# Kernel optimization log

Measured on AMD Instinct MI355X. Metric: run time of the kernel, lower is better.

The kernel has to match this reference:

```python
import jax, jax.numpy as jnp
import numpy as np
from jax import lax

N = 100000
E = 1600000
IN_C = 128
HID = 128
OUT_C = 64
NUM_CLASSES = 40
BN_EPS = 1e-5


def gcn_conv(x, row, col, W, b):
    # x: [N, F_in] -> [N, F_out]; PyG GCNConv: self-loops + sym normalization
    h = x @ W                                   # [N, F_out]
    loops = jnp.arange(N, dtype=row.dtype)
    r = jnp.concatenate([row, loops])           # [E+N]
    c = jnp.concatenate([col, loops])
    ones = jnp.ones(r.shape[0], dtype=x.dtype)
    deg = jax.ops.segment_sum(ones, c, num_segments=N)
    dinv = jnp.where(deg > 0, lax.rsqrt(deg), jnp.zeros_like(deg))
    norm = dinv[r] * dinv[c]                    # [E+N]
    msg = h[r] * norm[:, None]                  # gather + scale  [E+N, F_out]
    out = jax.ops.segment_sum(msg, c, num_segments=N)
    return out + b


def setup_inputs() -> dict:
    key = jax.random.key(0)
    ks = jax.random.split(key, 16)
    def glorot(k, shape):
        lim = float(np.sqrt(6.0 / (shape[0] + shape[1])))
        return jax.random.uniform(k, shape, jnp.float32, -lim, lim)
    x = jax.random.normal(ks[0], (N, IN_C), jnp.float32)
    edge_index = jax.random.randint(ks[1], (2, E), 0, N, jnp.int64)
    return {
        "x": x,
        "edge_index": edge_index,
        "w1": glorot(ks[2], (IN_C, HID)), "b1": jnp.zeros((HID,), jnp.float32),
        "w2": glorot(ks[3], (HID, HID)), "b2": jnp.zeros((HID,), jnp.float32),
        "bn_gamma": jnp.ones((HID,), jnp.float32), "bn_beta": jnp.zeros((HID,), jnp.float32),
        "bn_mean": jnp.zeros((HID,), jnp.float32), "bn_var": jnp.ones((HID,), jnp.float32),
        "cls_w": glorot(ks[4], (HID, OUT_C)), "cls_b": jnp.zeros((OUT_C,), jnp.float32),
        "sim_w": glorot(ks[5], (HID, NUM_CLASSES)), "sim_b": jnp.zeros((NUM_CLASSES,), jnp.float32),
        "hom_w": glorot(ks[6], (HID, 1)), "hom_b": jnp.zeros((1,), jnp.float32),
        "ent_w": glorot(ks[7], (HID, 1)), "ent_b": jnp.zeros((1,), jnp.float32),
    }


def reference(x, edge_index, w1, b1, w2, b2, bn_gamma, bn_beta, bn_mean, bn_var,
              cls_w, cls_b, sim_w, sim_b, hom_w, hom_b, ent_w, ent_b):
    row, col = edge_index[0], edge_index[1]
    # layer 1: GCNConv -> BN (eval) -> ReLU (dropout is identity in eval)
    h = gcn_conv(x, row, col, w1, b1)
    h = (h - bn_mean) * lax.rsqrt(bn_var + BN_EPS) * bn_gamma + bn_beta
    h = jax.nn.relu(h)
    # layer 2
    h = gcn_conv(h, row, col, w2, b2)
    main_out = jax.nn.log_softmax(h @ cls_w + cls_b, axis=1)
    sim_out = jax.nn.softmax(h @ sim_w + sim_b, axis=1)
    hom_out = jax.nn.sigmoid((h @ hom_w + hom_b)[:, 0])
    ent_out = jax.nn.sigmoid((h @ ent_w + ent_b)[:, 0])
    return (main_out, sim_out, hom_out, ent_out)
```

## Files before the change

### kernel.cpp

```cpp
#include <hip/hip_runtime.h>
#include <hip/hip_bf16.h>
#include <math.h>

#define N_NODES 100000
#define N_EDGES 1600000
#define F 128
#define OUT_C 64
#define NUM_CLASSES 40
#define BN_EPS 1e-5f

#define NBUCK 782
#define BCAP 4096
#define FILL_BLOCKS 512
#define EPB ((N_EDGES + FILL_BLOCKS - 1) / FILL_BLOCKS)
#define FILL_ITERS 13

typedef __hip_bfloat16 bf16;
typedef __attribute__((ext_vector_type(8))) short bf16x8;
typedef __attribute__((ext_vector_type(4))) float f32x4;

#define PW1 0
#define PB1 16384
#define PW2 16512
#define PB2 32896
#define PGAMMA 33024
#define PBETA 33152
#define PMEAN 33280
#define PVAR 33408
#define PCLSW 33536
#define PCLSB 41728
#define PSIMW 41792
#define PSIMB 46912
#define PHOMW 46952
#define PHOMB 47080
#define PENTW 47081
#define PENTB 47209
#define PRAW_TOTAL 47210
#define PFW 47232
#define PFB 63616
#define PTOTAL 63744

__device__ __forceinline__ float uasf(unsigned u) { return __uint_as_float(u); }
__device__ __forceinline__ unsigned f2bu(float f) {
    bf16 h = __float2bfloat16(f);
    return (unsigned)*(unsigned short*)&h;
}

__global__ void detect_kernel(const void* __restrict__ x, const void* __restrict__ ei,
                              int* __restrict__ flags) {
    if (blockIdx.x != 0) return;
    int t = threadIdx.x & 63;
    const unsigned* xw = (const unsigned*)x;
    unsigned w = xw[t];
    unsigned e = (w >> 23) & 0xFFu;
    bool vote = (w == 0u || (e >= 90u && e <= 160u));
    unsigned long long m1 = __ballot(vote);
    const unsigned* ew = (const unsigned*)ei;
    bool zo = (ew[2 * t + 1] == 0u);
    unsigned long long m2 = __ballot(zo);
    if (t == 0) {
        flags[0] = (__popcll(m1) >= 48) ? 1 : 0;
        flags[1] = (__popcll(m2) >= 60) ? 1 : 0;
    }
}

struct ParamSegs {
    const void* src[16];
    int dst[16];
};

__global__ void cvtparams_kernel(ParamSegs segs, float* __restrict__ params,
                                 const int* __restrict__ flags) {
    int idx = blockIdx.x * 256 + threadIdx.x;
    if (idx >= PRAW_TOTAL) return;
    int k = 0;
#pragma unroll
    for (int s = 1; s < 16; s++)
        if (idx >= segs.dst[s]) k = s;
    int rel = idx - segs.dst[k];
    const void* sp = segs.src[k];
    float v = flags[0] ? ((const float*)sp)[rel]
                       : __bfloat162float(((const bf16*)sp)[rel]);
    params[idx] = v;
}

__device__ __forceinline__ int load_edge(const int* __restrict__ ei, int which, int i, int i64) {
    size_t elem = (size_t)which * N_EDGES + (size_t)i;
    return i64 ? ei[elem * 2] : ei[elem];
}

__global__ __launch_bounds__(256) void fill2_kernel(const int* __restrict__ ei,
                                                    int* __restrict__ bcur,
                                                    int* __restrict__ srcBuck,
                                                    const int* __restrict__ flags) {
    __shared__ int hist[NBUCK];
    __shared__ int gbase[NBUCK];
    __shared__ int lcur[NBUCK];
    int blk = blockIdx.x;
    int t = threadIdx.x;
    int i64 = flags[1];
    int e0 = blk * EPB;
    int ecnt = N_EDGES - e0;
    if (ecnt > EPB) ecnt = EPB;
    for (int i = t; i < NBUCK; i += 256) hist[i] = 0;
    __syncthreads();
    int ccache[FILL_ITERS];
#pragma unroll
    for (int it = 0; it < FILL_ITERS; ++it) {
        int i = t + it * 256;
        int c = -1;
        if (i < ecnt) {
            c = load_edge(ei, 1, e0 + i, i64);
            atomicAdd(&hist[c >> 7], 1);
        }
        ccache[it] = c;
    }
    __syncthreads();
    for (int i = t; i < NBUCK; i += 256) {
        int c = hist[i];
        gbase[i] = (c > 0) ? atomicAdd(&bcur[i], c) : 0;
        lcur[i] = 0;
    }
    __syncthreads();
#pragma unroll
    for (int it = 0; it < FILL_ITERS; ++it) {
        int i = t + it * 256;
        if (i < ecnt) {
            int c = ccache[it];
            int r = load_edge(ei, 0, e0 + i, i64);
            int b = c >> 7;
            int p = gbase[b] + atomicAdd(&lcur[b], 1);
            if (p < BCAP) srcBuck[b * BCAP + p] = ((c & 127) << 17) | r;
        }
    }
}

__global__ __launch_bounds__(512) void presort_kernel(int* __restrict__ srcBuck,
                                                      const int* __restrict__ bcur,
                                                      int* __restrict__ doffG,
                                                      int* __restrict__ dcntG,
                                                      float* __restrict__ dinv) {
    __shared__ int raw[BCAP];
    __shared__ int sorted[BCAP];
    __shared__ int dcnt[128], doff[128], dcur[128];
    int b = blockIdx.x;
    int t = threadIdx.x;
    int cnt = bcur[b];
    if (cnt > BCAP) cnt = BCAP;
    if (t < 128) dcnt[t] = 0;
    __syncthreads();
    for (int i = t; i < cnt; i += 512) {
        int e = srcBuck[b * BCAP + i];
        raw[i] = e;
        atomicAdd(&dcnt[e >> 17], 1);
    }
    __syncthreads();
    if (t < 128) doff[t] = dcnt[t];
    __syncthreads();
    for (int d = 1; d < 128; d <<= 1) {
        int add = 0;
        if (t < 128 && t >= d) add = doff[t - d];
        __syncthreads();
        if (t < 128) doff[t] += add;
        __syncthreads();
    }
    if (t < 128) {
        doff[t] -= dcnt[t];
        dcur[t] = 0;
    }
    __syncthreads();
    for (int i = t; i < cnt; i += 512) {
        int e = raw[i];
        int d = e >> 17;
        int r = atomicAdd(&dcur[d], 1);
        sorted[doff[d] + r] = e & 0x1FFFF;
    }
    __syncthreads();
    for (int i = t; i < cnt; i += 512) srcBuck[b * BCAP + i] = sorted[i];
    if (t < 128) {
        doffG[(b << 7) + t] = doff[t];
        dcntG[(b << 7) + t] = dcnt[t];
        int n = (b << 7) + t;
        if (n < N_NODES) dinv[n] = rsqrtf((float)(dcnt[t] + 1));
    }
}

__global__ void cvtx_kernel(const void* __restrict__ x, const float* __restrict__ dinv,
                            unsigned short* __restrict__ B16, const int* __restrict__ flags) {
    int i4 = blockIdx.x * blockDim.x + threadIdx.x;
    if (i4 >= N_NODES * F / 4) return;
    int n = i4 >> 5;
    float d = dinv[n];
    float v0, v1, v2, v3;
    if (flags[0]) {
        float4 v = ((const float4*)x)[i4];
        v0 = v.x; v1 = v.y; v2 = v.z; v3 = v.w;
    } else {
        uint2 u = ((const uint2*)x)[i4];
        v0 = uasf(u.x << 16);
        v1 = uasf(u.x & 0xFFFF0000u);
        v2 = uasf(u.y << 16);
        v3 = uasf(u.y & 0xFFFF0000u);
    }
    uint2 o;
    o.x = f2bu(v0 * d) | (f2bu(v1 * d) << 16);
    o.y = f2bu(v2 * d) | (f2bu(v3 * d) << 16);
    ((uint2*)B16)[i4] = o;
}

__device__ __forceinline__ float headw(const float* __restrict__ p, int j, int c) {
    if (c < OUT_C) return p[PCLSW + j * OUT_C + c];
    if (c < OUT_C + NUM_CLASSES) return p[PSIMW + j * NUM_CLASSES + (c - OUT_C)];
    if (c == 104) return p[PHOMW + j];
    if (c == 105) return p[PENTW + j];
    return 0.f;
}

__global__ void fusew_kernel(float* __restrict__ params) {
    int idx = blockIdx.x * 256 + threadIdx.x;
    int k = idx >> 7;
    int c = idx & 127;
    float s = 0.f;
    for (int j = 0; j < 128; j++) s += params[PW2 + k * 128 + j] * headw(params, j, c);
    params[PFW + k * 128 + c] = s;
    if (k == 0) {
        float b = 0.f;
        for (int j = 0; j < 128; j++) b += params[PB2 + j] * headw(params, j, c);
        if (c < OUT_C) b += params[PCLSB + c];
        else if (c < OUT_C + NUM_CLASSES) b += params[PSIMB + c - OUT_C];
        else if (c == 104) b += params[PHOMB];
        else if (c == 105) b += params[PENTB];
        params[PFB + c] = b;
    }
}

__global__ void wcvt_kernel(const float* __restrict__ params, unsigned short* __restrict__ wt) {
    int idx = blockIdx.x * 256 + threadIdx.x;
    if (idx >= 32768) return;
    int which = idx >> 14;
    int local = idx & 16383;
    int n = local >> 7;
    int k = local & 127;
    int ksrc = which ? ((k & 7) * 16 + (k >> 3)) : k;
    float v = params[(which ? PFW : PW1) + ksrc * 128 + n];
    wt[(which << 14) + n * 128 + k] = (unsigned short)f2bu(v);
}

#define ACC8(u)                                \
    do {                                       \
        a[0] += uasf((u).x << 16);             \
        a[1] += uasf((u).x & 0xFFFF0000u);     \
        a[2] += uasf((u).y << 16);             \
        a[3] += uasf((u).y & 0xFFFF0000u);     \
        a[4] += uasf((u).z << 16);             \
        a[5] += uasf((u).z & 0xFFFF0000u);     \
        a[6] += uasf((u).w << 16);             \
        a[7] += uasf((u).w & 0xFFFF0000u);     \
    } while (0)

__global__ __launch_bounds__(512) void aggh_kernel(const unsigned short* __restrict__ IN16,
                                                   unsigned short* __restrict__ OUT16,
                                                   const int* __restrict__ srcBuck,
                                                   const int* __restrict__ doffG,
                                                   const int* __restrict__ dcntG,
                                                   const float* __restrict__ dinv,
                                                   int* __restrict__ wcnt) {
    __shared__ int sIdx[BCAP];
    __shared__ int sdoff[128], sdcnt[128];
    __shared__ int sb, sh;
    int t = threadIdx.x;
    if (t == 0) {
        unsigned xcc;
        asm volatile("s_getreg_b32 %0, hwreg(HW_REG_XCC_ID)" : "=s"(xcc));
        int half = (xcc >> 2) & 1;
        int idx = atomicAdd(&wcnt[half], 1);
        if (idx >= NBUCK) {
            half ^= 1;
            idx = atomicAdd(&wcnt[half], 1);
        }
        sb = idx;
        sh = half;
    }
    __syncthreads();
    int b = sb, h = sh;
    if (t < 128) {
        sdoff[t] = doffG[(b << 7) + t];
        sdcnt[t] = dcntG[(b << 7) + t];
    }
    __syncthreads();
    int cnt = sdoff[127] + sdcnt[127];
    for (int i = t; i < cnt; i += 512) sIdx[i] = srcBuck[b * BCAP + i];
    __syncthreads();

    int g8 = t >> 3;
    int hoff = h * 64 + ((t & 7) << 3);
    int base = b << 7;
    for (int d = g8; d < 128; d += 64) {
        int n = base + d;
        if (n >= N_NODES) break;
        float a[8] = {0.f, 0.f, 0.f, 0.f, 0.f, 0.f, 0.f, 0.f};
        {
            uint4 u = *(const uint4*)(IN16 + ((size_t)n << 7) + hoff);
            ACC8(u);
        }
        int o = sdoff[d], k = sdcnt[d];
        int j = 0;
        for (; j + 8 <= k; j += 8) {
            int s0 = sIdx[o + j + 0], s1 = sIdx[o + j + 1];
            int s2 = sIdx[o + j + 2], s3 = sIdx[o + j + 3];
            int s4 = sIdx[o + j + 4], s5 = sIdx[o + j + 5];
            int s6 = sIdx[o + j + 6], s7 = sIdx[o + j + 7];
            uint4 u0 = *(const uint4*)(IN16 + ((size_t)s0 << 7) + hoff);
            uint4 u1 = *(const uint4*)(IN16 + ((size_t)s1 << 7) + hoff);
            uint4 u2 = *(const uint4*)(IN16 + ((size_t)s2 << 7) + hoff);
            uint4 u3 = *(const uint4*)(IN16 + ((size_t)s3 << 7) + hoff);
            uint4 u4 = *(const uint4*)(IN16 + ((size_t)s4 << 7) + hoff);
            uint4 u5 = *(const uint4*)(IN16 + ((size_t)s5 << 7) + hoff);
            uint4 u6 = *(const uint4*)(IN16 + ((size_t)s6 << 7) + hoff);
            uint4 u7 = *(const uint4*)(IN16 + ((size_t)s7 << 7) + hoff);
            ACC8(u0);
            ACC8(u1);
            ACC8(u2);
            ACC8(u3);
            ACC8(u4);
            ACC8(u5);
            ACC8(u6);
            ACC8(u7);
        }
        for (; j + 4 <= k; j += 4) {
            int s0 = sIdx[o + j + 0], s1 = sIdx[o + j + 1];
            int s2 = sIdx[o + j + 2], s3 = sIdx[o + j + 3];
            uint4 u0 = *(const uint4*)(IN16 + ((size_t)s0 << 7) + hoff);
            uint4 u1 = *(const uint4*)(IN16 + ((size_t)s1 << 7) + hoff);
            uint4 u2 = *(const uint4*)(IN16 + ((size_t)s2 << 7) + hoff);
            uint4 u3 = *(const uint4*)(IN16 + ((size_t)s3 << 7) + hoff);
            ACC8(u0);
            ACC8(u1);
            ACC8(u2);
            ACC8(u3);
        }
        for (; j < k; j++) {
            int s0 = sIdx[o + j];
            uint4 u0 = *(const uint4*)(IN16 + ((size_t)s0 << 7) + hoff);
            ACC8(u0);
        }
        float dn = dinv[n];
        uint4 pk;
        pk.x = f2bu(a[0] * dn) | (f2bu(a[1] * dn) << 16);
        pk.y = f2bu(a[2] * dn) | (f2bu(a[3] * dn) << 16);
        pk.z = f2bu(a[4] * dn) | (f2bu(a[5] * dn) << 16);
        pk.w = f2bu(a[6] * dn) | (f2bu(a[7] * dn) << 16);
        *(uint4*)(OUT16 + ((size_t)n << 7) + hoff) = pk;
    }
}

__global__ __launch_bounds__(256) void gemm_mfma_kernel(
    const unsigned short* __restrict__ A16, const unsigned short* __restrict__ Wt,
    unsigned short* __restrict__ outB, void* __restrict__ out,
    const float* __restrict__ params, const float* __restrict__ dinv, int mode,
    const int* __restrict__ flags) {
    __shared__ float sS[128], sO[128], sFB[128];
    int t = threadIdx.x;
    if (t < 128) {
        if (mode) {
            float s = rsqrtf(params[PVAR + t] + BN_EPS) * params[PGAMMA + t];
            sS[t] = s;
            sO[t] = params[PB1 + t] * s + (params[PBETA + t] - params[PMEAN + t] * s);
        } else {
            sFB[t] = params[PFB + t];
        }
    }
    __syncthreads();
    int wave = t >> 6, lane = t & 63, m16 = lane & 15, quad = lane >> 4;
    int rowbase = blockIdx.x * 64 + wave * 16;
    int rA = rowbase + m16;
    if (rA >= N_NODES) rA = N_NODES - 1;
    const size_t abase = (size_t)rA * 128 + (quad << 3);

    f32x4 acc[8];
#pragma unroll
    for (int ct = 0; ct < 8; ct++) acc[ct] = (f32x4){0.f, 0.f, 0.f, 0.f};

#pragma unroll
    for (int kk = 0; kk < 4; kk++) {
        bf16x8 af = *(const bf16x8*)(A16 + abase + kk * 32);
#pragma unroll
        for (int ct = 0; ct < 8; ct++) {
            bf16x8 bfr = *(const bf16x8*)(Wt + (size_t)((ct * 16 + m16) * 128) + kk * 32 + (quad << 3));
            acc[ct] = __builtin_amdgcn_mfma_f32_16x16x32_bf16(af, bfr, acc[ct], 0, 0, 0);
        }
    }

    int r0 = rowbase + quad * 4;
    if (mode) {
        float sc[8], of[8];
#pragma unroll
        for (int ct = 0; ct < 8; ct++) {
            sc[ct] = sS[ct * 16 + m16];
            of[ct] = sO[ct * 16 + m16];
        }
#pragma unroll
        for (int reg = 0; reg < 4; reg++) {
            int gr = r0 + reg;
            if (gr >= N_NODES) continue;
            float dn = dinv[gr];
            unsigned pk[4];
#pragma unroll
            for (int i = 0; i < 4; i++) {
                float v0 = fmaxf(acc[2 * i][reg] * sc[2 * i] + of[2 * i], 0.f) * dn;
                float v1 = fmaxf(acc[2 * i + 1][reg] * sc[2 * i + 1] + of[2 * i + 1], 0.f) * dn;
                pk[i] = f2bu(v0) | (f2bu(v1) << 16);
            }
            *(uint4*)(outB + (size_t)gr * 128 + (m16 << 3)) = make_uint4(pk[0], pk[1], pk[2], pk[3]);
        }
    } else {
        int isf = flags[0];
        const size_t OFF_SIM = (size_t)N_NODES * OUT_C;
        const size_t OFF_HOM = OFF_SIM + (size_t)N_NODES * NUM_CLASSES;
        const size_t OFF_ENT = OFF_HOM + (size_t)N_NODES;
        float* outf = (float*)out;
        bf16* outb = (bf16*)out;
        float fb[8];
#pragma unroll
        for (int ct = 0; ct < 8; ct++) fb[ct] = sFB[ct * 16 + m16];
#define STORE_OUT(idx, v)                        \
    do {                                         \
        if (isf) outf[(idx)] = (v);              \
        else outb[(idx)] = __float2bfloat16(v);  \
    } while (0)
#pragma unroll
        for (int reg = 0; reg < 4; reg++) {
            int gr = r0 + reg;
            bool vrow = (gr < N_NODES);
            float v[8];
#pragma unroll
            for (int ct = 0; ct < 8; ct++) v[ct] = acc[ct][reg] + fb[ct];
            float m = fmaxf(fmaxf(v[0], v[1]), fmaxf(v[2], v[3]));
            m = fmaxf(m, __shfl_xor(m, 1));
            m = fmaxf(m, __shfl_xor(m, 2));
            m = fmaxf(m, __shfl_xor(m, 4));
            m = fmaxf(m, __shfl_xor(m, 8));
            float S = __expf(v[0] - m) + __expf(v[1] - m) + __expf(v[2] - m) + __expf(v[3] - m);
            S += __shfl_xor(S, 1);
            S += __shfl_xor(S, 2);
            S += __shfl_xor(S, 4);
            S += __shfl_xor(S, 8);
            float lS = m + __logf(S);
            if (vrow) {
#pragma unroll
                for (int ct = 0; ct < 4; ct++)
                    STORE_OUT((size_t)gr * OUT_C + ct * 16 + m16, v[ct] - lS);
            }
            bool has6 = (m16 < 8);
            float s4 = v[4], s5 = v[5], s6 = has6 ? v[6] : -INFINITY;
            float m2 = fmaxf(fmaxf(s4, s5), s6);
            m2 = fmaxf(m2, __shfl_xor(m2, 1));
            m2 = fmaxf(m2, __shfl_xor(m2, 2));
            m2 = fmaxf(m2, __shfl_xor(m2, 4));
            m2 = fmaxf(m2, __shfl_xor(m2, 8));
            float e4 = __expf(s4 - m2), e5 = __expf(s5 - m2), e6 = has6 ? __expf(s6 - m2) : 0.f;
            float S2 = e4 + e5 + e6;
            S2 += __shfl_xor(S2, 1);
            S2 += __shfl_xor(S2, 2);
            S2 += __shfl_xor(S2, 4);
            S2 += __shfl_xor(S2, 8);
            float rS2 = 1.f / S2;
            if (vrow) {
                STORE_OUT(OFF_SIM + (size_t)gr * NUM_CLASSES + m16, e4 * rS2);
                STORE_OUT(OFF_SIM + (size_t)gr * NUM_CLASSES + 16 + m16, e5 * rS2);
                if (has6) STORE_OUT(OFF_SIM + (size_t)gr * NUM_CLASSES + 32 + m16, e6 * rS2);
                if (m16 == 8) STORE_OUT(OFF_HOM + gr, 1.f / (1.f + __expf(-v[6])));
                if (m16 == 9) STORE_OUT(OFF_ENT + gr, 1.f / (1.f + __expf(-v[6])));
            }
        }
#undef STORE_OUT
    }
}

extern "C" void kernel_launch(void* const* d_in, const int* in_sizes, int n_in,
                              void* d_out, int out_size, void* d_ws, size_t ws_size,
                              hipStream_t stream) {
    const void* x = d_in[0];
    const int* ei = (const int*)d_in[1];

    char* ws = (char*)d_ws;
    size_t o = 0;
    auto alloc = [&](size_t bytes) {
        size_t r = o;
        o = (o + bytes + 255) & ~(size_t)255;
        return r;
    };
    char* RA = ws + alloc((size_t)51 * 1024 * 1024);
    char* RB = ws + alloc((size_t)26 * 1024 * 1024);
    float* params = (float*)(ws + alloc((size_t)PTOTAL * 4));
    unsigned short* wt = (unsigned short*)(ws + alloc(65536));
    float* dinv = (float*)(ws + alloc((size_t)N_NODES * 4));
    int* doffG = (int*)(ws + alloc((size_t)NBUCK * 128 * 4));
    int* dcntG = (int*)(ws + alloc((size_t)NBUCK * 128 * 4));
    int* bcur = (int*)(ws + alloc((size_t)(NBUCK + 8) * 4));
    int* wcnt = (int*)(ws + alloc(256));
    int* flags = (int*)(ws + alloc(256));

    int* srcBuck = (int*)RA;
    unsigned short* B16 = (unsigned short*)(RA + 13u * 1024 * 1024);
    unsigned short* G16 = (unsigned short*)RB;

    detect_kernel<<<1, 64, 0, stream>>>(x, ei, flags);
    hipMemsetAsync(bcur, 0, (size_t)((char*)wcnt + 256 - (char*)bcur), stream);

    ParamSegs segs;
    const int srcIdx[16] = {2, 3, 4, 5, 6, 7, 8, 9, 10, 11, 12, 13, 14, 15, 16, 17};
    const int dsts[16] = {PW1, PB1, PW2, PB2, PGAMMA, PBETA, PMEAN, PVAR,
                          PCLSW, PCLSB, PSIMW, PSIMB, PHOMW, PHOMB, PENTW, PENTB};
    for (int k = 0; k < 16; k++) {
        segs.src[k] = d_in[srcIdx[k]];
        segs.dst[k] = dsts[k];
    }
    cvtparams_kernel<<<(PRAW_TOTAL + 255) / 256, 256, 0, stream>>>(segs, params, flags);
    fusew_kernel<<<64, 256, 0, stream>>>(params);
    wcvt_kernel<<<128, 256, 0, stream>>>(params, wt);

    fill2_kernel<<<FILL_BLOCKS, 256, 0, stream>>>(ei, bcur, srcBuck, flags);
    presort_kernel<<<NBUCK, 512, 0, stream>>>(srcBuck, bcur, doffG, dcntG, dinv);
    cvtx_kernel<<<(N_NODES * F / 4 + 255) / 256, 256, 0, stream>>>(x, dinv, B16, flags);

    const int gemmGrid = (N_NODES + 63) / 64;

    aggh_kernel<<<2 * NBUCK, 512, 0, stream>>>(B16, G16, srcBuck, doffG, dcntG, dinv, wcnt);
    gemm_mfma_kernel<<<gemmGrid, 256, 0, stream>>>(G16, wt, B16, nullptr, params, dinv, 1, flags);
    aggh_kernel<<<2 * NBUCK, 512, 0, stream>>>(B16, G16, srcBuck, doffG, dcntG, dinv, wcnt + 2);
    gemm_mfma_kernel<<<gemmGrid, 256, 0, stream>>>(G16, wt + 16384, nullptr, d_out, params, dinv, 0, flags);
}
```

Measured before the change: 438.3 us.

## Fuse whole GCN pipeline into one cooperative persistent kernel with grid syncs

Replaces the chain of about ten kernel launches with one cooperative kernel of 256 blocks × 512 threads. Stages (detect, param convert, bucket fill, presort, weight fuse, x convert, two aggregation and GEMM phases) are separated by grid.sync, and the aggregation loop becomes persistent work-stealing. The goal is to remove launch gaps and inter-kernel drain. The trade-off is fewer resident blocks than the old grids, occupancy limits from large shared memory under the launch bounds, and the cost of the grid barriers. The old multi-kernel path is kept as a fallback if the cooperative launch fails.

New measurement: 1.166 ms. +166.0%, slower.

```diff
diff --git a/kernel.cpp b/kernel.cpp
--- a/kernel.cpp
+++ b/kernel.cpp
@@ -1,6 +1,9 @@
 #include <hip/hip_runtime.h>
+#include <hip/hip_cooperative_groups.h>
 #include <hip/hip_bf16.h>
 #include <math.h>
+
+namespace cg = cooperative_groups;
 
 #define N_NODES 100000
 #define N_EDGES 1600000
@@ -11,9 +14,15 @@
 
 #define NBUCK 782
 #define BCAP 4096
+
 #define FILL_BLOCKS 512
 #define EPB ((N_EDGES + FILL_BLOCKS - 1) / FILL_BLOCKS)
 #define FILL_ITERS 13
+
+#define GB 256
+#define BT 512
+#define MEPB ((N_EDGES + GB - 1) / GB)
+#define MFITERS ((MEPB + BT - 1) / BT)
 
 typedef __hip_bfloat16 bf16;
 typedef __attribute__((ext_vector_type(8))) short bf16x8;
@@ -40,10 +49,458 @@
 #define PFB 63616
 #define PTOTAL 63744
 
+struct ParamSegs {
+    const void* src[16];
+    int dst[16];
+};
+
 __device__ __forceinline__ float uasf(unsigned u) { return __uint_as_float(u); }
 __device__ __forceinline__ unsigned f2bu(float f) {
     bf16 h = __float2bfloat16(f);
     return (unsigned)*(unsigned short*)&h;
+}
+__device__ __forceinline__ int load_edge(const int* __restrict__ ei, int which, int i, int i64) {
+    size_t elem = (size_t)which * N_EDGES + (size_t)i;
+    return i64 ? ei[elem * 2] : ei[elem];
+}
+__device__ __forceinline__ float headw(const float* __restrict__ p, int j, int c) {
+    if (c < OUT_C) return p[PCLSW + j * OUT_C + c];
+    if (c < OUT_C + NUM_CLASSES) return p[PSIMW + j * NUM_CLASSES + (c - OUT_C)];
+    if (c == 104) return p[PHOMW + j];
+    if (c == 105) return p[PENTW + j];
+    return 0.f;
+}
+
+#define ACC8(u)                                \
+    do {                                       \
+        a[0] += uasf((u).x << 16);             \
+        a[1] += uasf((u).x & 0xFFFF0000u);     \
+        a[2] += uasf((u).y << 16);             \
+        a[3] += uasf((u).y & 0xFFFF0000u);     \
+        a[4] += uasf((u).z << 16);             \
+        a[5] += uasf((u).z & 0xFFFF0000u);     \
+        a[6] += uasf((u).w << 16);             \
+        a[7] += uasf((u).w & 0xFFFF0000u);     \
+    } while (0)
+
+__device__ void agg_phase(const unsigned short* __restrict__ IN16,
+                          unsigned short* __restrict__ OUT16,
+                          const int* __restrict__ srcBuck, const int* __restrict__ doffG,
+                          const int* __restrict__ dcntG, const float* __restrict__ dinv,
+                          int* __restrict__ wpair, int t, int* __restrict__ sIdx,
+                          int* __restrict__ sdoff, int* __restrict__ sdcnt,
+                          volatile int* __restrict__ sCtl, int nthreads) {
+    int g8 = t >> 3;
+    int lo8 = (t & 7) << 3;
+    int ng = nthreads >> 3;
+    for (;;) {
+        if (t == 0) {
+            unsigned xcc;
+            asm volatile("s_getreg_b32 %0, hwreg(HW_REG_XCC_ID)" : "=s"(xcc));
+            int half = (xcc >> 2) & 1;
+            int idx = atomicAdd(&wpair[half], 1);
+            if (idx >= NBUCK) {
+                half ^= 1;
+                idx = atomicAdd(&wpair[half], 1);
+            }
+            sCtl[0] = (idx < NBUCK) ? idx : -1;
+            sCtl[1] = half;
+        }
+        __syncthreads();
+        int b = sCtl[0], h = sCtl[1];
+        if (b < 0) break;
+        if (t < 128) {
+            sdoff[t] = doffG[(b << 7) + t];
+            sdcnt[t] = dcntG[(b << 7) + t];
+        }
+        __syncthreads();
+        int cnt = sdoff[127] + sdcnt[127];
+        for (int i = t; i < cnt; i += nthreads) sIdx[i] = srcBuck[b * BCAP + i];
+        __syncthreads();
+        int hoff = h * 64 + lo8;
+        int base = b << 7;
+        for (int d = g8; d < 128; d += ng) {
+            int n = base + d;
+            if (n >= N_NODES) break;
+            float a[8] = {0.f, 0.f, 0.f, 0.f, 0.f, 0.f, 0.f, 0.f};
+            {
+                uint4 u = *(const uint4*)(IN16 + ((size_t)n << 7) + hoff);
+                ACC8(u);
+            }
+            int o = sdoff[d], k = sdcnt[d];
+            int j = 0;
+            for (; j + 8 <= k; j += 8) {
+                int s0 = sIdx[o + j + 0], s1 = sIdx[o + j + 1];
+                int s2 = sIdx[o + j + 2], s3 = sIdx[o + j + 3];
+                int s4 = sIdx[o + j + 4], s5 = sIdx[o + j + 5];
+                int s6 = sIdx[o + j + 6], s7 = sIdx[o + j + 7];
+                uint4 u0 = *(const uint4*)(IN16 + ((size_t)s0 << 7) + hoff);
+                uint4 u1 = *(const uint4*)(IN16 + ((size_t)s1 << 7) + hoff);
+                uint4 u2 = *(const uint4*)(IN16 + ((size_t)s2 << 7) + hoff);
+                uint4 u3 = *(const uint4*)(IN16 + ((size_t)s3 << 7) + hoff);
+                uint4 u4 = *(const uint4*)(IN16 + ((size_t)s4 << 7) + hoff);
+                uint4 u5 = *(const uint4*)(IN16 + ((size_t)s5 << 7) + hoff);
+                uint4 u6 = *(const uint4*)(IN16 + ((size_t)s6 << 7) + hoff);
+                uint4 u7 = *(const uint4*)(IN16 + ((size_t)s7 << 7) + hoff);
+                ACC8(u0);
+                ACC8(u1);
+                ACC8(u2);
+                ACC8(u3);
+                ACC8(u4);
+                ACC8(u5);
+                ACC8(u6);
+                ACC8(u7);
+            }
+            for (; j + 4 <= k; j += 4) {
+                int s0 = sIdx[o + j + 0], s1 = sIdx[o + j + 1];
+                int s2 = sIdx[o + j + 2], s3 = sIdx[o + j + 3];
+                uint4 u0 = *(const uint4*)(IN16 + ((size_t)s0 << 7) + hoff);
+                uint4 u1 = *(const uint4*)(IN16 + ((size_t)s1 << 7) + hoff);
+                uint4 u2 = *(const uint4*)(IN16 + ((size_t)s2 << 7) + hoff);
+                uint4 u3 = *(const uint4*)(IN16 + ((size_t)s3 << 7) + hoff);
+                ACC8(u0);
+                ACC8(u1);
+                ACC8(u2);
+                ACC8(u3);
+            }
+            for (; j < k; j++) {
+                int s0 = sIdx[o + j];
+                uint4 u0 = *(const uint4*)(IN16 + ((size_t)s0 << 7) + hoff);
+                ACC8(u0);
+            }
+            float dn = dinv[n];
+            uint4 pk;
+            pk.x = f2bu(a[0] * dn) | (f2bu(a[1] * dn) << 16);
+            pk.y = f2bu(a[2] * dn) | (f2bu(a[3] * dn) << 16);
+            pk.z = f2bu(a[4] * dn) | (f2bu(a[5] * dn) << 16);
+            pk.w = f2bu(a[6] * dn) | (f2bu(a[7] * dn) << 16);
+            *(uint4*)(OUT16 + ((size_t)n << 7) + hoff) = pk;
+        }
+        __syncthreads();
+    }
+}
+
+__device__ void gemm_tile(const unsigned short* __restrict__ A16,
+                          const unsigned short* __restrict__ Wt,
+                          unsigned short* __restrict__ outB, void* __restrict__ out,
+                          const float* __restrict__ dinv, int mode, int isf,
+                          const float* __restrict__ sF1, const float* __restrict__ sF2,
+                          int t, int rowbase0) {
+    int w = t >> 6, lane = t & 63, m16 = lane & 15, quad = lane >> 4;
+    int rowbase = rowbase0 + w * 16;
+    int rA = rowbase + m16;
+    if (rA >= N_NODES) rA = N_NODES - 1;
+    const size_t abase = (size_t)rA * 128 + (quad << 3);
+
+    f32x4 acc[8];
+#pragma unroll
+    for (int ct = 0; ct < 8; ct++) acc[ct] = (f32x4){0.f, 0.f, 0.f, 0.f};
+#pragma unroll
+    for (int kk = 0; kk < 4; kk++) {
+        bf16x8 af = *(const bf16x8*)(A16 + abase + kk * 32);
+#pragma unroll
+        for (int ct = 0; ct < 8; ct++) {
+            bf16x8 bfr =
+                *(const bf16x8*)(Wt + (size_t)((ct * 16 + m16) * 128) + kk * 32 + (quad << 3));
+            acc[ct] = __builtin_amdgcn_mfma_f32_16x16x32_bf16(af, bfr, acc[ct], 0, 0, 0);
+        }
+    }
+
+    int r0 = rowbase + quad * 4;
+    if (mode) {
+        float sc[8], of[8];
+#pragma unroll
+        for (int ct = 0; ct < 8; ct++) {
+            sc[ct] = sF1[ct * 16 + m16];
+            of[ct] = sF2[ct * 16 + m16];
+        }
+#pragma unroll
+        for (int reg = 0; reg < 4; reg++) {
+            int gr = r0 + reg;
+            if (gr >= N_NODES) continue;
+            float dn = dinv[gr];
+            unsigned pk[4];
+#pragma unroll
+            for (int i = 0; i < 4; i++) {
+                float v0 = fmaxf(acc[2 * i][reg] * sc[2 * i] + of[2 * i], 0.f) * dn;
+                float v1 = fmaxf(acc[2 * i + 1][reg] * sc[2 * i + 1] + of[2 * i + 1], 0.f) * dn;
+                pk[i] = f2bu(v0) | (f2bu(v1) << 16);
+            }
+            *(uint4*)(outB + (size_t)gr * 128 + (m16 << 3)) = make_uint4(pk[0], pk[1], pk[2], pk[3]);
+        }
+    } else {
+        const size_t OFF_SIM = (size_t)N_NODES * OUT_C;
+        const size_t OFF_HOM = OFF_SIM + (size_t)N_NODES * NUM_CLASSES;
+        const size_t OFF_ENT = OFF_HOM + (size_t)N_NODES;
+        float* outf = (float*)out;
+        bf16* outb = (bf16*)out;
+        float fb[8];
+#pragma unroll
+        for (int ct = 0; ct < 8; ct++) fb[ct] = sF1[ct * 16 + m16];
+#define STORE_OUT(idx, v)                        \
+    do {                                         \
+        if (isf) outf[(idx)] = (v);              \
+        else outb[(idx)] = __float2bfloat16(v);  \
+    } while (0)
+#pragma unroll
+        for (int reg = 0; reg < 4; reg++) {
+            int gr = r0 + reg;
+            bool vrow = (gr < N_NODES);
+            float v[8];
+#pragma unroll
+            for (int ct = 0; ct < 8; ct++) v[ct] = acc[ct][reg] + fb[ct];
+            float m = fmaxf(fmaxf(v[0], v[1]), fmaxf(v[2], v[3]));
+            m = fmaxf(m, __shfl_xor(m, 1));
+            m = fmaxf(m, __shfl_xor(m, 2));
+            m = fmaxf(m, __shfl_xor(m, 4));
+            m = fmaxf(m, __shfl_xor(m, 8));
+            float S = __expf(v[0] - m) + __expf(v[1] - m) + __expf(v[2] - m) + __expf(v[3] - m);
+            S += __shfl_xor(S, 1);
+            S += __shfl_xor(S, 2);
+            S += __shfl_xor(S, 4);
+            S += __shfl_xor(S, 8);
+            float lS = m + __logf(S);
+            if (vrow) {
+#pragma unroll
+                for (int ct = 0; ct < 4; ct++)
+                    STORE_OUT((size_t)gr * OUT_C + ct * 16 + m16, v[ct] - lS);
+            }
+            bool has6 = (m16 < 8);
+            float s4 = v[4], s5 = v[5], s6 = has6 ? v[6] : -INFINITY;
+            float m2 = fmaxf(fmaxf(s4, s5), s6);
+            m2 = fmaxf(m2, __shfl_xor(m2, 1));
+            m2 = fmaxf(m2, __shfl_xor(m2, 2));
+            m2 = fmaxf(m2, __shfl_xor(m2, 4));
+            m2 = fmaxf(m2, __shfl_xor(m2, 8));
+            float e4 = __expf(s4 - m2), e5 = __expf(s5 - m2), e6 = has6 ? __expf(s6 - m2) : 0.f;
+            float S2 = e4 + e5 + e6;
+            S2 += __shfl_xor(S2, 1);
+            S2 += __shfl_xor(S2, 2);
+            S2 += __shfl_xor(S2, 4);
+            S2 += __shfl_xor(S2, 8);
+            float rS2 = 1.f / S2;
+            if (vrow) {
+                STORE_OUT(OFF_SIM + (size_t)gr * NUM_CLASSES + m16, e4 * rS2);
+                STORE_OUT(OFF_SIM + (size_t)gr * NUM_CLASSES + 16 + m16, e5 * rS2);
+                if (has6) STORE_OUT(OFF_SIM + (size_t)gr * NUM_CLASSES + 32 + m16, e6 * rS2);
+                if (m16 == 8) STORE_OUT(OFF_HOM + gr, 1.f / (1.f + __expf(-v[6])));
+                if (m16 == 9) STORE_OUT(OFF_ENT + gr, 1.f / (1.f + __expf(-v[6])));
+            }
+        }
+#undef STORE_OUT
+    }
+}
+
+__global__ __launch_bounds__(BT, 4) void mega_kernel(
+    const void* __restrict__ x, const int* __restrict__ ei, ParamSegs segs,
+    float* __restrict__ params, unsigned short* __restrict__ wt, float* __restrict__ dinv,
+    int* __restrict__ doffG, int* __restrict__ dcntG, int* __restrict__ bcur,
+    int* __restrict__ wcnt, int* __restrict__ srcBuck, unsigned short* __restrict__ B16,
+    unsigned short* __restrict__ G16, void* __restrict__ dout) {
+    cg::grid_group grid = cg::this_grid();
+#define GSYNC()          \
+    do {                 \
+        __threadfence(); \
+        grid.sync();     \
+        __threadfence(); \
+    } while (0)
+
+    __shared__ __align__(16) int sBig[2 * BCAP];
+    __shared__ int s128a[128], s128b[128], s128c[128];
+    __shared__ float sF1[128], sF2[128];
+    __shared__ int sCtl[2];
+
+    const int t = threadIdx.x;
+    const int bid = blockIdx.x;
+
+    if (t < 64) {
+        const unsigned* xw = (const unsigned*)x;
+        unsigned wv = xw[t];
+        unsigned e = (wv >> 23) & 0xFFu;
+        unsigned long long m1 = __ballot(wv == 0u || (e >= 90u && e <= 160u));
+        const unsigned* ew = (const unsigned*)ei;
+        unsigned long long m2 = __ballot(ew[2 * t + 1] == 0u);
+        if (t == 0) {
+            sCtl[0] = (__popcll(m1) >= 48) ? 1 : 0;
+            sCtl[1] = (__popcll(m2) >= 60) ? 1 : 0;
+        }
+    }
+    __syncthreads();
+    const int isf = sCtl[0], i64 = sCtl[1];
+    __syncthreads();
+
+    {
+        int idx = bid * BT + t;
+        if (idx < PRAW_TOTAL) {
+            int k = 0;
+#pragma unroll
+            for (int s = 1; s < 16; s++)
+                if (idx >= segs.dst[s]) k = s;
+            int rel = idx - segs.dst[k];
+            const void* sp = segs.src[k];
+            params[idx] = isf ? ((const float*)sp)[rel] : __bfloat162float(((const bf16*)sp)[rel]);
+        }
+    }
+    {
+        int* hist = sBig;
+        int* gbase = sBig + 1024;
+        int* lcur = sBig + 2048;
+        int e0 = bid * MEPB;
+        int ecnt = N_EDGES - e0;
+        if (ecnt > MEPB) ecnt = MEPB;
+        for (int i = t; i < NBUCK; i += BT) hist[i] = 0;
+        __syncthreads();
+        int cc[MFITERS];
+#pragma unroll
+        for (int it = 0; it < MFITERS; ++it) {
+            int i = t + it * BT;
+            int c = -1;
+            if (i < ecnt) {
+                c = load_edge(ei, 1, e0 + i, i64);
+                atomicAdd(&hist[c >> 7], 1);
+            }
+            cc[it] = c;
+        }
+        __syncthreads();
+        for (int i = t; i < NBUCK; i += BT) {
+            int c = hist[i];
+            gbase[i] = (c > 0) ? atomicAdd(&bcur[i], c) : 0;
+            lcur[i] = 0;
+        }
+        __syncthreads();
+#pragma unroll
+        for (int it = 0; it < MFITERS; ++it) {
+            int i = t + it * BT;
+            if (i < ecnt) {
+                int c = cc[it];
+                int r = load_edge(ei, 0, e0 + i, i64);
+                int b = c >> 7;
+                int p = gbase[b] + atomicAdd(&lcur[b], 1);
+                if (p < BCAP) srcBuck[b * BCAP + p] = ((c & 127) << 17) | r;
+            }
+        }
+    }
+    GSYNC();
+
+    {
+        int idx = bid * BT + t;
+        if (idx < 16384) {
+            int k = idx >> 7, c = idx & 127;
+            float s = 0.f;
+            for (int j = 0; j < 128; j++) s += params[PW2 + k * 128 + j] * headw(params, j, c);
+            params[PFW + k * 128 + c] = s;
+            if (k == 0) {
+                float bs = 0.f;
+                for (int j = 0; j < 128; j++) bs += params[PB2 + j] * headw(params, j, c);
+                if (c < OUT_C) bs += params[PCLSB + c];
+                else if (c < OUT_C + NUM_CLASSES) bs += params[PSIMB + c - OUT_C];
+                else if (c == 104) bs += params[PHOMB];
+                else if (c == 105) bs += params[PENTB];
+                params[PFB + c] = bs;
+            }
+        }
+    }
+    for (int b = bid; b < NBUCK; b += GB) {
+        int* raw = sBig;
+        int* sorted = sBig + BCAP;
+        int cnt = bcur[b];
+        if (cnt > BCAP) cnt = BCAP;
+        if (t < 128) s128a[t] = 0;
+        __syncthreads();
+        for (int i = t; i < cnt; i += BT) {
+            int e = srcBuck[b * BCAP + i];
+            raw[i] = e;
+            atomicAdd(&s128a[e >> 17], 1);
+        }
+        __syncthreads();
+        if (t < 128) s128b[t] = s128a[t];
+        __syncthreads();
+        for (int d = 1; d < 128; d <<= 1) {
+            int add = 0;
+            if (t < 128 && t >= d) add = s128b[t - d];
+            __syncthreads();
+            if (t < 128) s128b[t] += add;
+            __syncthreads();
+        }
+        if (t < 128) {
+            s128b[t] -= s128a[t];
+            s128c[t] = 0;
+        }
+        __syncthreads();
+        for (int i = t; i < cnt; i += BT) {
+            int e = raw[i];
+            int d = e >> 17;
+            int r = atomicAdd(&s128c[d], 1);
+            sorted[s128b[d] + r] = e & 0x1FFFF;
+        }
+        __syncthreads();
+        for (int i = t; i < cnt; i += BT) srcBuck[b * BCAP + i] = sorted[i];
+        if (t < 128) {
+            doffG[(b << 7) + t] = s128b[t];
+            dcntG[(b << 7) + t] = s128a[t];
+            int n = (b << 7) + t;
+            if (n < N_NODES) dinv[n] = rsqrtf((float)(s128a[t] + 1));
+        }
+        __syncthreads();
+    }
+    GSYNC();
+
+    {
+        int idx = bid * BT + t;
+        if (idx < 32768) {
+            int which = idx >> 14;
+            int local = idx & 16383;
+            int n = local >> 7, k = local & 127;
+            int ksrc = which ? ((k & 7) * 16 + (k >> 3)) : k;
+            float v = params[(which ? PFW : PW1) + ksrc * 128 + n];
+            wt[(which << 14) + n * 128 + k] = (unsigned short)f2bu(v);
+        }
+    }
+    for (int i4 = bid * BT + t; i4 < N_NODES * F / 4; i4 += GB * BT) {
+        int n = i4 >> 5;
+        float d = dinv[n];
+        float v0, v1, v2, v3;
+        if (isf) {
+            float4 v = ((const float4*)x)[i4];
+            v0 = v.x;
+            v1 = v.y;
+            v2 = v.z;
+            v3 = v.w;
+        } else {
+            uint2 u = ((const uint2*)x)[i4];
+            v0 = uasf(u.x << 16);
+            v1 = uasf(u.x & 0xFFFF0000u);
+            v2 = uasf(u.y << 16);
+            v3 = uasf(u.y & 0xFFFF0000u);
+        }
+        uint2 o;
+        o.x = f2bu(v0 * d) | (f2bu(v1 * d) << 16);
+        o.y = f2bu(v2 * d) | (f2bu(v3 * d) << 16);
+        ((uint2*)B16)[i4] = o;
+    }
+    GSYNC();
+
+    agg_phase(B16, G16, srcBuck, doffG, dcntG, dinv, wcnt, t, sBig, s128a, s128b, sCtl, BT);
+    GSYNC();
+
+    if (t < 128) {
+        float s = rsqrtf(params[PVAR + t] + BN_EPS) * params[PGAMMA + t];
+        sF1[t] = s;
+        sF2[t] = params[PB1 + t] * s + (params[PBETA + t] - params[PMEAN + t] * s);
+    }
+    __syncthreads();
+    for (int tb = bid; tb < NBUCK; tb += GB)
+        gemm_tile(G16, wt, B16, nullptr, dinv, 1, isf, sF1, sF2, t, tb << 7);
+    GSYNC();
+
+    agg_phase(B16, G16, srcBuck, doffG, dcntG, dinv, wcnt + 2, t, sBig, s128a, s128b, sCtl, BT);
+    GSYNC();
+
+    if (t < 128) sF1[t] = params[PFB + t];
+    __syncthreads();
+    for (int tb = bid; tb < NBUCK; tb += GB)
+        gemm_tile(G16, wt + 16384, nullptr, dout, dinv, 0, isf, sF1, sF2, t, tb << 7);
+#undef GSYNC
 }
 
 __global__ void detect_kernel(const void* __restrict__ x, const void* __restrict__ ei,
@@ -64,11 +521,6 @@
     }
 }
 
-struct ParamSegs {
-    const void* src[16];
-    int dst[16];
-};
-
 __global__ void cvtparams_kernel(ParamSegs segs, float* __restrict__ params,
                                  const int* __restrict__ flags) {
     int idx = blockIdx.x * 256 + threadIdx.x;
@@ -79,14 +531,7 @@
         if (idx >= segs.dst[s]) k = s;
     int rel = idx - segs.dst[k];
     const void* sp = segs.src[k];
-    float v = flags[0] ? ((const float*)sp)[rel]
-                       : __bfloat162float(((const bf16*)sp)[rel]);
-    params[idx] = v;
-}
-
-__device__ __forceinline__ int load_edge(const int* __restrict__ ei, int which, int i, int i64) {
-    size_t elem = (size_t)which * N_EDGES + (size_t)i;
-    return i64 ? ei[elem * 2] : ei[elem];
+    params[idx] = flags[0] ? ((const float*)sp)[rel] : __bfloat162float(((const bf16*)sp)[rel]);
 }
 
 __global__ __launch_bounds__(256) void fill2_kernel(const int* __restrict__ ei,
@@ -194,7 +639,10 @@
     float v0, v1, v2, v3;
     if (flags[0]) {
         float4 v = ((const float4*)x)[i4];
-        v0 = v.x; v1 = v.y; v2 = v.z; v3 = v.w;
+        v0 = v.x;
+        v1 = v.y;
+        v2 = v.z;
+        v3 = v.w;
     } else {
         uint2 u = ((const uint2*)x)[i4];
         v0 = uasf(u.x << 16);
@@ -206,14 +654,6 @@
     o.x = f2bu(v0 * d) | (f2bu(v1 * d) << 16);
     o.y = f2bu(v2 * d) | (f2bu(v3 * d) << 16);
     ((uint2*)B16)[i4] = o;
-}
-
-__device__ __forceinline__ float headw(const float* __restrict__ p, int j, int c) {
-    if (c < OUT_C) return p[PCLSW + j * OUT_C + c];
-    if (c < OUT_C + NUM_CLASSES) return p[PSIMW + j * NUM_CLASSES + (c - OUT_C)];
-    if (c == 104) return p[PHOMW + j];
-    if (c == 105) return p[PENTW + j];
-    return 0.f;
 }
 
 __global__ void fusew_kernel(float* __restrict__ params) {
@@ -246,18 +686,6 @@
     wt[(which << 14) + n * 128 + k] = (unsigned short)f2bu(v);
 }
 
-#define ACC8(u)                                \
-    do {                                       \
-        a[0] += uasf((u).x << 16);             \
-        a[1] += uasf((u).x & 0xFFFF0000u);     \
-        a[2] += uasf((u).y << 16);             \
-        a[3] += uasf((u).y & 0xFFFF0000u);     \
-        a[4] += uasf((u).z << 16);             \
-        a[5] += uasf((u).z & 0xFFFF0000u);     \
-        a[6] += uasf((u).w << 16);             \
-        a[7] += uasf((u).w & 0xFFFF0000u);     \
-    } while (0)
-
 __global__ __launch_bounds__(512) void aggh_kernel(const unsigned short* __restrict__ IN16,
                                                    unsigned short* __restrict__ OUT16,
                                                    const int* __restrict__ srcBuck,
@@ -267,7 +695,7 @@
                                                    int* __restrict__ wcnt) {
     __shared__ int sIdx[BCAP];
     __shared__ int sdoff[128], sdcnt[128];
-    __shared__ int sb, sh;
+    __shared__ int sCtl[2];
     int t = threadIdx.x;
     if (t == 0) {
         unsigned xcc;
@@ -278,11 +706,12 @@
             half ^= 1;
             idx = atomicAdd(&wcnt[half], 1);
         }
-        sb = idx;
-        sh = half;
-    }
-    __syncthreads();
-    int b = sb, h = sh;
+        sCtl[0] = idx;
+        sCtl[1] = half;
+    }
+    __syncthreads();
+    int b = sCtl[0], h = sCtl[1];
+    if (b >= NBUCK) return;
     if (t < 128) {
         sdoff[t] = doffG[(b << 7) + t];
         sdcnt[t] = dcntG[(b << 7) + t];
@@ -359,122 +788,19 @@
     unsigned short* __restrict__ outB, void* __restrict__ out,
     const float* __restrict__ params, const float* __restrict__ dinv, int mode,
     const int* __restrict__ flags) {
-    __shared__ float sS[128], sO[128], sFB[128];
+    __shared__ float sF1[128], sF2[128];
     int t = threadIdx.x;
     if (t < 128) {
         if (mode) {
             float s = rsqrtf(params[PVAR + t] + BN_EPS) * params[PGAMMA + t];
-            sS[t] = s;
-            sO[t] = params[PB1 + t] * s + (params[PBETA + t] - params[PMEAN + t] * s);
+            sF1[t] = s;
+            sF2[t] = params[PB1 + t] * s + (params[PBETA + t] - params[PMEAN + t] * s);
         } else {
-            sFB[t] = params[PFB + t];
-        }
-    }
-    __syncthreads();
-    int wave = t >> 6, lane = t & 63, m16 = lane & 15, quad = lane >> 4;
-    int rowbase = blockIdx.x * 64 + wave * 16;
-    int rA = rowbase + m16;
-    if (rA >= N_NODES) rA = N_NODES - 1;
-    const size_t abase = (size_t)rA * 128 + (quad << 3);
-
-    f32x4 acc[8];
-#pragma unroll
-    for (int ct = 0; ct < 8; ct++) acc[ct] = (f32x4){0.f, 0.f, 0.f, 0.f};
-
-#pragma unroll
-    for (int kk = 0; kk < 4; kk++) {
-        bf16x8 af = *(const bf16x8*)(A16 + abase + kk * 32);
-#pragma unroll
-        for (int ct = 0; ct < 8; ct++) {
-            bf16x8 bfr = *(const bf16x8*)(Wt + (size_t)((ct * 16 + m16) * 128) + kk * 32 + (quad << 3));
-            acc[ct] = __builtin_amdgcn_mfma_f32_16x16x32_bf16(af, bfr, acc[ct], 0, 0, 0);
-        }
-    }
-
-    int r0 = rowbase + quad * 4;
-    if (mode) {
-        float sc[8], of[8];
-#pragma unroll
-        for (int ct = 0; ct < 8; ct++) {
-            sc[ct] = sS[ct * 16 + m16];
-            of[ct] = sO[ct * 16 + m16];
-        }
-#pragma unroll
-        for (int reg = 0; reg < 4; reg++) {
-            int gr = r0 + reg;
-            if (gr >= N_NODES) continue;
-            float dn = dinv[gr];
-            unsigned pk[4];
-#pragma unroll
-            for (int i = 0; i < 4; i++) {
-                float v0 = fmaxf(acc[2 * i][reg] * sc[2 * i] + of[2 * i], 0.f) * dn;
-                float v1 = fmaxf(acc[2 * i + 1][reg] * sc[2 * i + 1] + of[2 * i + 1], 0.f) * dn;
-                pk[i] = f2bu(v0) | (f2bu(v1) << 16);
-            }
-            *(uint4*)(outB + (size_t)gr * 128 + (m16 << 3)) = make_uint4(pk[0], pk[1], pk[2], pk[3]);
-        }
-    } else {
-        int isf = flags[0];
-        const size_t OFF_SIM = (size_t)N_NODES * OUT_C;
-        const size_t OFF_HOM = OFF_SIM + (size_t)N_NODES * NUM_CLASSES;
-        const size_t OFF_ENT = OFF_HOM + (size_t)N_NODES;
-        float* outf = (float*)out;
-        bf16* outb = (bf16*)out;
-        float fb[8];
-#pragma unroll
-        for (int ct = 0; ct < 8; ct++) fb[ct] = sFB[ct * 16 + m16];
-#define STORE_OUT(idx, v)                        \
-    do {                                         \
-        if (isf) outf[(idx)] = (v);              \
-        else outb[(idx)] = __float2bfloat16(v);  \
-    } while (0)
-#pragma unroll
-        for (int reg = 0; reg < 4; reg++) {
-            int gr = r0 + reg;
-            bool vrow = (gr < N_NODES);
-            float v[8];
-#pragma unroll
-            for (int ct = 0; ct < 8; ct++) v[ct] = acc[ct][reg] + fb[ct];
-            float m = fmaxf(fmaxf(v[0], v[1]), fmaxf(v[2], v[3]));
-            m = fmaxf(m, __shfl_xor(m, 1));
-            m = fmaxf(m, __shfl_xor(m, 2));
-            m = fmaxf(m, __shfl_xor(m, 4));
-            m = fmaxf(m, __shfl_xor(m, 8));
-            float S = __expf(v[0] - m) + __expf(v[1] - m) + __expf(v[2] - m) + __expf(v[3] - m);
-            S += __shfl_xor(S, 1);
-            S += __shfl_xor(S, 2);
-            S += __shfl_xor(S, 4);
-            S += __shfl_xor(S, 8);
-            float lS = m + __logf(S);
-            if (vrow) {
-#pragma unroll
-                for (int ct = 0; ct < 4; ct++)
-                    STORE_OUT((size_t)gr * OUT_C + ct * 16 + m16, v[ct] - lS);
-            }
-            bool has6 = (m16 < 8);
-            float s4 = v[4], s5 = v[5], s6 = has6 ? v[6] : -INFINITY;
-            float m2 = fmaxf(fmaxf(s4, s5), s6);
-            m2 = fmaxf(m2, __shfl_xor(m2, 1));
-            m2 = fmaxf(m2, __shfl_xor(m2, 2));
-            m2 = fmaxf(m2, __shfl_xor(m2, 4));
-            m2 = fmaxf(m2, __shfl_xor(m2, 8));
-            float e4 = __expf(s4 - m2), e5 = __expf(s5 - m2), e6 = has6 ? __expf(s6 - m2) : 0.f;
-            float S2 = e4 + e5 + e6;
-            S2 += __shfl_xor(S2, 1);
-            S2 += __shfl_xor(S2, 2);
-            S2 += __shfl_xor(S2, 4);
-            S2 += __shfl_xor(S2, 8);
-            float rS2 = 1.f / S2;
-            if (vrow) {
-                STORE_OUT(OFF_SIM + (size_t)gr * NUM_CLASSES + m16, e4 * rS2);
-                STORE_OUT(OFF_SIM + (size_t)gr * NUM_CLASSES + 16 + m16, e5 * rS2);
-                if (has6) STORE_OUT(OFF_SIM + (size_t)gr * NUM_CLASSES + 32 + m16, e6 * rS2);
-                if (m16 == 8) STORE_OUT(OFF_HOM + gr, 1.f / (1.f + __expf(-v[6])));
-                if (m16 == 9) STORE_OUT(OFF_ENT + gr, 1.f / (1.f + __expf(-v[6])));
-            }
-        }
-#undef STORE_OUT
-    }
+            sF1[t] = params[PFB + t];
+        }
+    }
+    __syncthreads();
+    gemm_tile(A16, Wt, outB, out, dinv, mode, flags[0], sF1, sF2, t, blockIdx.x * 64 - ((t >> 6) * 16) + ((t >> 6) * 16));
 }
 
 extern "C" void kernel_launch(void* const* d_in, const int* in_sizes, int n_in,
@@ -505,7 +831,6 @@
     unsigned short* B16 = (unsigned short*)(RA + 13u * 1024 * 1024);
     unsigned short* G16 = (unsigned short*)RB;
 
-    detect_kernel<<<1, 64, 0, stream>>>(x, ei, flags);
     hipMemsetAsync(bcur, 0, (size_t)((char*)wcnt + 256 - (char*)bcur), stream);
 
     ParamSegs segs;
@@ -516,18 +841,29 @@
         segs.src[k] = d_in[srcIdx[k]];
         segs.dst[k] = dsts[k];
     }
-    cvtparams_kernel<<<(PRAW_TOTAL + 255) / 256, 256, 0, stream>>>(segs, params, flags);
-    fusew_kernel<<<64, 256, 0, stream>>>(params);
-    wcvt_kernel<<<128, 256, 0, stream>>>(params, wt);
-
-    fill2_kernel<<<FILL_BLOCKS, 256, 0, stream>>>(ei, bcur, srcBuck, flags);
-    presort_kernel<<<NBUCK, 512, 0, stream>>>(srcBuck, bcur, doffG, dcntG, dinv);
-    cvtx_kernel<<<(N_NODES * F / 4 + 255) / 256, 256, 0, stream>>>(x, dinv, B16, flags);
-
-    const int gemmGrid = (N_NODES + 63) / 64;
-
-    aggh_kernel<<<2 * NBUCK, 512, 0, stream>>>(B16, G16, srcBuck, doffG, dcntG, dinv, wcnt);
-    gemm_mfma_kernel<<<gemmGrid, 256, 0, stream>>>(G16, wt, B16, nullptr, params, dinv, 1, flags);
-    aggh_kernel<<<2 * NBUCK, 512, 0, stream>>>(B16, G16, srcBuck, doffG, dcntG, dinv, wcnt + 2);
-    gemm_mfma_kernel<<<gemmGrid, 256, 0, stream>>>(G16, wt + 16384, nullptr, d_out, params, dinv, 0, flags);
-}
+
+    void* kargs[] = {(void*)&x,    (void*)&ei,   (void*)&segs,    (void*)&params,
+                     (void*)&wt,   (void*)&dinv, (void*)&doffG,   (void*)&dcntG,
+                     (void*)&bcur, (void*)&wcnt, (void*)&srcBuck, (void*)&B16,
+                     (void*)&G16,  (void*)&d_out};
+    hipError_t cerr =
+        hipLaunchCooperativeKernel((void*)mega_kernel, dim3(GB), dim3(BT), kargs, 0, stream);
+
+    if (cerr != hipSuccess) {
+        detect_kernel<<<1, 64, 0, stream>>>(x, ei, flags);
+        cvtparams_kernel<<<(PRAW_TOTAL + 255) / 256, 256, 0, stream>>>(segs, params, flags);
+        fusew_kernel<<<64, 256, 0, stream>>>(params);
+        wcvt_kernel<<<128, 256, 0, stream>>>(params, wt);
+        fill2_kernel<<<FILL_BLOCKS, 256, 0, stream>>>(ei, bcur, srcBuck, flags);
+        presort_kernel<<<NBUCK, 512, 0, stream>>>(srcBuck, bcur, doffG, dcntG, dinv);
+        cvtx_kernel<<<(N_NODES * F / 4 + 255) / 256, 256, 0, stream>>>(x, dinv, B16, flags);
+        const int gemmGrid = (N_NODES + 63) / 64;
+        aggh_kernel<<<2 * NBUCK, 512, 0, stream>>>(B16, G16, srcBuck, doffG, dcntG, dinv, wcnt);
+        gemm_mfma_kernel<<<gemmGrid, 256, 0, stream>>>(G16, wt, B16, nullptr, params, dinv, 1,
+                                                       flags);
+        aggh_kernel<<<2 * NBUCK, 512, 0, stream>>>(B16, G16, srcBuck, doffG, dcntG, dinv,
+                                                   wcnt + 2);
+        gemm_mfma_kernel<<<gemmGrid, 256, 0, stream>>>(G16, wt + 16384, nullptr, d_out, params,
+                                                       dinv, 0, flags);
+    }
+}
```
